# Kernel optimization log

Measured on AMD Instinct MI355X. Metric: run time of the kernel, lower is better.

The kernel has to match this reference:

```python
import jax, jax.numpy as jnp
import numpy as np

B, T, F, U, M, OUT = 2048, 16, 512, 512, 8, 3
DELTA_T = 0.04
EPS = 1e-07


def setup_inputs() -> dict:
    key = jax.random.key(0)
    ks = jax.random.split(key, 6)
    s_in = 1.0 / np.sqrt(F + U)
    s_u = 1.0 / np.sqrt(U)
    return {
        "x": jax.random.normal(ks[0], (B, T, F), dtype=jnp.float32),
        "W_r": jax.random.normal(ks[1], (F + U, U * M), dtype=jnp.float32) * s_in,
        "b_r": jnp.zeros((U * M,), dtype=jnp.float32),
        "W_q": jax.random.normal(ks[2], (F + U, U), dtype=jnp.float32) * s_in,
        "b_q": jnp.zeros((U,), dtype=jnp.float32),
        "W_s": jax.random.normal(ks[3], (F + U, U * M), dtype=jnp.float32) * s_in,
        "b_s": jnp.zeros((U * M,), dtype=jnp.float32),
        "W_o": jax.random.normal(ks[4], (U, OUT), dtype=jnp.float32) * s_u,
        "b_o": jnp.zeros((OUT,), dtype=jnp.float32),
    }


def _ln_tau_table():
    # tau_i = 10^(i/2)  =>  ln tau_i = i * 0.5 * ln(10)
    return (jnp.arange(M, dtype=jnp.float32) * (0.5 * np.log(10.0)))


def reference(x, W_r, b_r, W_q, b_q, W_s, b_s, W_o, b_o):
    ln_tau = _ln_tau_table()                       # (M,)
    decay = jnp.exp(-DELTA_T / (jnp.exp(ln_tau) + EPS))  # (M,)

    def step(h_hat, x_t):
        # h_hat: (B, U, M), x_t: (B, F)
        h = h_hat.sum(axis=2)                       # (B, U)
        fi = jnp.concatenate([x_t, h], axis=1)      # (B, F+U)
        ln_r = (fi @ W_r + b_r).reshape(-1, U, M)
        r = jax.nn.softmax(-jnp.square(ln_r - ln_tau), axis=2)
        ctx = jnp.sum(r * h_hat, axis=2)            # (B, U)
        q = jnp.tanh(jnp.concatenate([x_t, ctx], axis=1) @ W_q + b_q)[:, :, None]
        ln_s = (fi @ W_s + b_s).reshape(-1, U, M)
        s = jax.nn.softmax(-jnp.square(ln_s - ln_tau), axis=2)
        h_hat_next = ((1.0 - s) * h_hat + s * q) * decay
        hidden = h_hat_next.sum(axis=2)             # (B, U)
        return h_hat_next, hidden

    h0 = jnp.zeros((x.shape[0], U, M), dtype=x.dtype)
    xs = jnp.swapaxes(x, 0, 1)                      # (T, B, F)
    _, hs = jax.lax.scan(step, h0, xs)              # hs: (T, B, U)
    hs = jnp.swapaxes(hs, 0, 1)                     # (B, T, U)
    out = hs @ W_o + b_o                            # (B, T, OUT)
    return out
```

## Files before the change

### kernel.cpp

```cpp
#include <hip/hip_runtime.h>
#include <math.h>

#define B_ 2048
#define T_ 16
#define F_ 512
#define U_ 512
#define M_ 8

typedef _Float16 half8 __attribute__((ext_vector_type(8)));
typedef float f32x4 __attribute__((ext_vector_type(4)));

__device__ __forceinline__ void load_lds16(const _Float16* gsrc, _Float16* lds) {
    __builtin_amdgcn_global_load_lds(
        (const __attribute__((address_space(1))) void*)gsrc,
        (__attribute__((address_space(3))) void*)lds, 16, 0, 0);
}

#define BAR() __builtin_amdgcn_s_barrier()
#define LGKM0() asm volatile("s_waitcnt lgkmcnt(0)" ::: "memory")
#define VMW(n) asm volatile("s_waitcnt vmcnt(" #n ")" ::: "memory")
#define MFMA16(a, b, c) __builtin_amdgcn_mfma_f32_16x16x32_f16(a, b, c, 0, 0, 0)

struct Decay8 { float d[8]; };

__global__ __launch_bounds__(256) void cast_x_kernel(const float* __restrict__ in,
                                                     _Float16* __restrict__ out) {
    long i = (long)blockIdx.x * 256 + threadIdx.x;
    const f32x4* p = (const f32x4*)in;
    f32x4 a = p[i * 2], b = p[i * 2 + 1];
    half8 v;
    v[0] = (_Float16)a[0]; v[1] = (_Float16)a[1]; v[2] = (_Float16)a[2]; v[3] = (_Float16)a[3];
    v[4] = (_Float16)b[0]; v[5] = (_Float16)b[1]; v[6] = (_Float16)b[2]; v[7] = (_Float16)b[3];
    ((half8*)out)[i] = v;
}

__global__ __launch_bounds__(256) void transpose_cast_kernel(const float* __restrict__ W,
                                                             _Float16* __restrict__ Wt,
                                                             int K, int N) {
    __shared__ float tile[32][33];
    int n0 = blockIdx.x * 32, k0 = blockIdx.y * 32;
    int tx = threadIdx.x, ty = threadIdx.y;
    #pragma unroll
    for (int i = 0; i < 32; i += 8)
        tile[ty + i][tx] = W[(long)(k0 + ty + i) * N + n0 + tx];
    __syncthreads();
    #pragma unroll
    for (int i = 0; i < 32; i += 8)
        Wt[(long)(n0 + ty + i) * K + k0 + tx] = (_Float16)tile[tx][ty + i];
}

__global__ __launch_bounds__(256) void transpose_cast_perm_kernel(const float* __restrict__ W,
                                                                  _Float16* __restrict__ Wt,
                                                                  int rowbase) {
    const int K = 1024, N = 4096;
    __shared__ float tile[32][33];
    int n0 = blockIdx.x * 32, k0 = blockIdx.y * 32;
    int tx = threadIdx.x, ty = threadIdx.y;
    #pragma unroll
    for (int i = 0; i < 32; i += 8)
        tile[ty + i][tx] = W[(long)(k0 + ty + i) * N + n0 + tx];
    __syncthreads();
    #pragma unroll
    for (int i = 0; i < 32; i += 8) {
        int nl = n0 + ty + i;
        int u = nl >> 3, m = nl & 7;
        int nn = ((u >> 4) << 7) + (m << 4) + (u & 15);
        Wt[(long)(rowbase + nn) * K + k0 + tx] = (_Float16)tile[tx][ty + i];
    }
}

__global__ __launch_bounds__(512, 2) void gemm1_fused_kernel(
    const _Float16* __restrict__ A0, long lda0,
    const _Float16* __restrict__ A1, long lda1,
    const _Float16* __restrict__ Wt,
    const float* __restrict__ b_r, const float* __restrict__ b_s,
    const _Float16* __restrict__ h_hat,
    _Float16* __restrict__ ctx,
    _Float16* __restrict__ s_buf) {
    constexpr int NT = 16;
    const float LT = 1.1512925464970228f;
    __shared__ __align__(16) _Float16 As[2][256 * 64];
    __shared__ __align__(16) _Float16 Bs[2][256 * 64];
    const int tid = threadIdx.x;
    const int lane = tid & 63;
    const int wave = tid >> 6;
    const int wm = wave >> 1, wn = wave & 1;
    const int l15 = lane & 15, lhi = lane >> 4, swz = lane & 7;
    const int g0 = (lhi ^ swz) * 8;
    const int g1 = ((lhi + 4) ^ swz) * 8;
    const int srow = tid >> 3;
    const int sg = (tid & 7) ^ (srow & 7);
    const int ldsdst = wave * 64 * 8;
    const long m0 = (long)blockIdx.y * 256;
    const long n0 = (long)blockIdx.x * 256;

#define STAGE_A(kt_, buf_, r_) do {                                             \
        int kt__ = (kt_);                                                       \
        const _Float16* s_; long lda_; int kofs_;                               \
        if (kt__ < 8) { s_ = A0; lda_ = lda0; kofs_ = kt__ * 64; }              \
        else          { s_ = A1; lda_ = lda1; kofs_ = kt__ * 64 - 512; }        \
        load_lds16(s_ + (m0 + (r_) * 64 + srow) * lda_ + kofs_ + sg * 8,        \
                   &As[buf_][(r_) * 4096 + ldsdst]);                            \
    } while (0)
#define STAGE_B(kt_, buf_, r_)                                                  \
        load_lds16(Wt + (n0 + (r_) * 64 + srow) * 1024 + (kt_) * 64 + sg * 8,   \
                   &Bs[buf_][(r_) * 4096 + ldsdst])

    f32x4 acc[4][8] = {};

    #pragma unroll
    for (int r = 0; r < 4; ++r) STAGE_A(0, 0, r);
    #pragma unroll
    for (int r = 0; r < 4; ++r) STAGE_B(0, 0, r);
    #pragma unroll
    for (int r = 0; r < 4; ++r) STAGE_A(1, 1, r);
    STAGE_B(1, 1, 0); STAGE_B(1, 1, 2);
    VMW(6);
    BAR();

    #pragma unroll 1
    for (int t = 0; t < NT; ++t) {
        const int cur = t & 1, nxt = cur ^ 1;
        const _Float16* Ac = &As[cur][0];
        const _Float16* Bc = &Bs[cur][0];
        half8 af[4][2], bfa[2][2], bfb[2][2];

        #pragma unroll
        for (int i = 0; i < 4; ++i) {
            const _Float16* p = Ac + (wm * 64 + i * 16 + l15) * 64;
            af[i][0] = *(const half8*)(p + g0);
            af[i][1] = *(const half8*)(p + g1);
        }
        #pragma unroll
        for (int j = 0; j < 2; ++j) {
            const _Float16* p = Bc + (wn * 128 + j * 16 + l15) * 64;
            bfa[j][0] = *(const half8*)(p + g0);
            bfa[j][1] = *(const half8*)(p + g1);
        }
        if (t + 1 < NT) { STAGE_B(t + 1, nxt, 1); STAGE_B(t + 1, nxt, 3); }
        BAR(); LGKM0();
        __builtin_amdgcn_s_setprio(1);
        #pragma unroll
        for (int i = 0; i < 4; ++i)
            #pragma unroll
            for (int j = 0; j < 2; ++j) {
                acc[i][j] = MFMA16(af[i][0], bfa[j][0], acc[i][j]);
                acc[i][j] = MFMA16(af[i][1], bfa[j][1], acc[i][j]);
            }
        __builtin_amdgcn_s_setprio(0);
        BAR();

        #pragma unroll
        for (int j = 0; j < 2; ++j) {
            const _Float16* p = Bc + (wn * 128 + (2 + j) * 16 + l15) * 64;
            bfb[j][0] = *(const half8*)(p + g0);
            bfb[j][1] = *(const half8*)(p + g1);
        }
        if (t + 2 < NT) { STAGE_A(t + 2, cur, 0); STAGE_A(t + 2, cur, 1); }
        BAR(); LGKM0();
        __builtin_amdgcn_s_setprio(1);
        #pragma unroll
        for (int i = 0; i < 4; ++i)
            #pragma unroll
            for (int j = 0; j < 2; ++j) {
                acc[i][2 + j] = MFMA16(af[i][0], bfb[j][0], acc[i][2 + j]);
                acc[i][2 + j] = MFMA16(af[i][1], bfb[j][1], acc[i][2 + j]);
            }
        __builtin_amdgcn_s_setprio(0);
        BAR();

        #pragma unroll
        for (int j = 0; j < 2; ++j) {
            const _Float16* p = Bc + (wn * 128 + (4 + j) * 16 + l15) * 64;
            bfa[j][0] = *(const half8*)(p + g0);
            bfa[j][1] = *(const half8*)(p + g1);
        }
        if (t + 2 < NT) { STAGE_A(t + 2, cur, 2); STAGE_A(t + 2, cur, 3); }
        BAR(); LGKM0();
        __builtin_amdgcn_s_setprio(1);
        #pragma unroll
        for (int i = 0; i < 4; ++i)
            #pragma unroll
            for (int j = 0; j < 2; ++j) {
                acc[i][4 + j] = MFMA16(af[i][0], bfa[j][0], acc[i][4 + j]);
                acc[i][4 + j] = MFMA16(af[i][1], bfa[j][1], acc[i][4 + j]);
            }
        __builtin_amdgcn_s_setprio(0);
        BAR();

        #pragma unroll
        for (int j = 0; j < 2; ++j) {
            const _Float16* p = Bc + (wn * 128 + (6 + j) * 16 + l15) * 64;
            bfb[j][0] = *(const half8*)(p + g0);
            bfb[j][1] = *(const half8*)(p + g1);
        }
        if (t + 2 < NT) { STAGE_B(t + 2, cur, 0); STAGE_B(t + 2, cur, 2); }
        LGKM0();
        __builtin_amdgcn_s_setprio(1);
        #pragma unroll
        for (int i = 0; i < 4; ++i)
            #pragma unroll
            for (int j = 0; j < 2; ++j) {
                acc[i][6 + j] = MFMA16(af[i][0], bfb[j][0], acc[i][6 + j]);
                acc[i][6 + j] = MFMA16(af[i][1], bfb[j][1], acc[i][6 + j]);
            }
        __builtin_amdgcn_s_setprio(0);
        if (t + 2 < NT)      { VMW(6); }
        else if (t + 1 < NT) { VMW(0); }
        BAR();
    }

    const int r4 = lhi * 4;
    const int panel = (int)(n0 >> 7) + wn;
    const bool is_r = panel < 32;
    const int u = (is_r ? panel : panel - 32) * 16 + l15;
    const float* bias = is_r ? b_r : b_s;
    f32x4 bl0 = *(const f32x4*)(bias + u * 8);
    f32x4 bl1 = *(const f32x4*)(bias + u * 8 + 4);

    #pragma unroll
    for (int i = 0; i < 4; ++i) {
        #pragma unroll
        for (int r = 0; r < 4; ++r) {
            long m = m0 + wm * 64 + i * 16 + r4 + r;
            float z[8]; float zmax = -1e30f;
            #pragma unroll
            for (int j = 0; j < 8; ++j) {
                float v = acc[i][j][r] + (j < 4 ? bl0[j] : bl1[j - 4]);
                float d = v - (float)j * LT;
                z[j] = -d * d;
                zmax = fmaxf(zmax, z[j]);
            }
            float e[8]; float se = 0.f;
            #pragma unroll
            for (int j = 0; j < 8; ++j) { e[j] = __expf(z[j] - zmax); se += e[j]; }
            float inv = 1.f / se;
            if (is_r) {
                half8 hh = *(const half8*)(h_hat + m * 4096 + u * 8);
                float c = 0.f;
                #pragma unroll
                for (int j = 0; j < 8; ++j) c += e[j] * (float)hh[j];
                ctx[m * 512 + u] = (_Float16)(c * inv);
            } else {
                half8 sv;
                #pragma unroll
                for (int j = 0; j < 8; ++j) sv[j] = (_Float16)(e[j] * inv);
                *(half8*)(s_buf + m * 4096 + u * 8) = sv;
            }
        }
    }
#undef STAGE_A
#undef STAGE_B
}

__global__ __launch_bounds__(256) void gemm2_fused_kernel(
    const _Float16* __restrict__ A0, long lda0,
    const _Float16* __restrict__ A1, long lda1,
    const _Float16* __restrict__ Wt,
    const float* __restrict__ bias,
    const _Float16* __restrict__ s_buf,
    _Float16* __restrict__ h_hat,
    _Float16* __restrict__ hs_t,
    Decay8 dec) {
    constexpr int BM = 64, BN = 64, FM = 2, FN = 2;
    __shared__ __align__(16) _Float16 As[BM * 64];
    __shared__ __align__(16) _Float16 Bs[BN * 64];
    const int tid = threadIdx.x;
    const int lane = tid & 63;
    const int wave = tid >> 6;
    const int wm = wave >> 1, wn = wave & 1;
    const long m0 = (long)blockIdx.y * BM;
    const long n0 = (long)blockIdx.x * BN;

    f32x4 acc[FM][FN] = {};

    for (int kt = 0; kt < 16; ++kt) {
        const _Float16* Asrc; long lda; int kofs;
        if (kt < 8) { Asrc = A0; lda = lda0; kofs = kt * 64; }
        else        { Asrc = A1; lda = lda1; kofs = kt * 64 - 512; }
        #pragma unroll
        for (int c = 0; c < 2; ++c) {
            int idx = c * 256 + tid;
            int row = idx >> 3, g = idx & 7;
            int gsrc = g ^ (row & 7);
            load_lds16(Asrc + (m0 + row) * lda + kofs + gsrc * 8,
                       As + (c * 256 + (wave << 6)) * 8);
        }
        #pragma unroll
        for (int c = 0; c < 2; ++c) {
            int idx = c * 256 + tid;
            int row = idx >> 3, g = idx & 7;
            int gsrc = g ^ (row & 7);
            load_lds16(Wt + (n0 + row) * 1024 + kt * 64 + gsrc * 8,
                       Bs + (c * 256 + (wave << 6)) * 8);
        }
        __syncthreads();
        #pragma unroll
        for (int ks = 0; ks < 2; ++ks) {
            half8 af[FM], bf[FN];
            #pragma unroll
            for (int i = 0; i < FM; ++i) {
                int row = wm * 32 + i * 16 + (lane & 15);
                int g = ks * 4 + (lane >> 4);
                int gs = g ^ (row & 7);
                af[i] = *(const half8*)(As + row * 64 + gs * 8);
            }
            #pragma unroll
            for (int j = 0; j < FN; ++j) {
                int row = wn * 32 + j * 16 + (lane & 15);
                int g = ks * 4 + (lane >> 4);
                int gs = g ^ (row & 7);
                bf[j] = *(const half8*)(Bs + row * 64 + gs * 8);
            }
            #pragma unroll
            for (int i = 0; i < FM; ++i)
                #pragma unroll
                for (int j = 0; j < FN; ++j)
                    acc[i][j] = MFMA16(af[i], bf[j], acc[i][j]);
        }
        __syncthreads();
    }

    const int r4 = (lane >> 4) * 4;
    const int c16 = lane & 15;
    #pragma unroll
    for (int i = 0; i < FM; ++i) {
        #pragma unroll
        for (int j = 0; j < FN; ++j) {
            #pragma unroll
            for (int r = 0; r < 4; ++r) {
                long b = m0 + wm * 32 + i * 16 + r4 + r;
                long u = n0 + wn * 32 + j * 16 + c16;
                float q = tanhf(acc[i][j][r] + bias[u]);
                half8 s8 = *(const half8*)(s_buf + b * 4096 + u * 8);
                half8 h8 = *(const half8*)(h_hat + b * 4096 + u * 8);
                half8 hn;
                float hval = 0.f;
                #pragma unroll
                for (int m = 0; m < 8; ++m) {
                    float sm = (float)s8[m];
                    float x = ((1.f - sm) * (float)h8[m] + sm * q) * dec.d[m];
                    hn[m] = (_Float16)x;
                    hval += x;
                }
                *(half8*)(h_hat + b * 4096 + u * 8) = hn;
                hs_t[b * 512 + u] = (_Float16)hval;
            }
        }
    }
}

__global__ __launch_bounds__(64) void out_proj_kernel(const _Float16* __restrict__ hs,
                                                      const float* __restrict__ W_o,
                                                      const float* __restrict__ b_o,
                                                      float* __restrict__ out) {
    const int bt = blockIdx.x;
    const int t = bt >> 11, b = bt & 2047;
    const int lane = threadIdx.x;
    half8 v = *(const half8*)(hs + ((long)t * 2048 + b) * 512 + lane * 8);
    float p0 = 0.f, p1 = 0.f, p2 = 0.f;
    #pragma unroll
    for (int m = 0; m < 8; ++m) {
        float hv = (float)v[m];
        int u = lane * 8 + m;
        p0 += hv * W_o[u * 3 + 0];
        p1 += hv * W_o[u * 3 + 1];
        p2 += hv * W_o[u * 3 + 2];
    }
    #pragma unroll
    for (int s = 32; s > 0; s >>= 1) {
        p0 += __shfl_down(p0, s);
        p1 += __shfl_down(p1, s);
        p2 += __shfl_down(p2, s);
    }
    if (lane == 0) {
        long o = ((long)b * T_ + t) * 3;
        out[o + 0] = p0 + b_o[0];
        out[o + 1] = p1 + b_o[1];
        out[o + 2] = p2 + b_o[2];
    }
}

extern "C" void kernel_launch(void* const* d_in, const int* in_sizes, int n_in,
                              void* d_out, int out_size, void* d_ws, size_t ws_size,
                              hipStream_t stream) {
    const float* x   = (const float*)d_in[0];
    const float* W_r = (const float*)d_in[1];
    const float* b_r = (const float*)d_in[2];
    const float* W_q = (const float*)d_in[3];
    const float* b_q = (const float*)d_in[4];
    const float* W_s = (const float*)d_in[5];
    const float* b_s = (const float*)d_in[6];
    const float* W_o = (const float*)d_in[7];
    const float* b_o = (const float*)d_in[8];
    float* out = (float*)d_out;

    char* ws = (char*)d_ws;
    size_t off = 0;
    _Float16* x_h   = (_Float16*)(ws + off); off += (size_t)B_ * T_ * F_ * 2;
    _Float16* Wrs_t = (_Float16*)(ws + off); off += (size_t)8192 * 1024 * 2;
    _Float16* Wq_t  = (_Float16*)(ws + off); off += (size_t)512 * 1024 * 2;
    _Float16* s_buf = (_Float16*)(ws + off); off += (size_t)B_ * 4096 * 2;
    _Float16* h_hat = (_Float16*)(ws + off); off += (size_t)B_ * 4096 * 2;
    _Float16* ctx_h = (_Float16*)(ws + off); off += (size_t)B_ * U_ * 2;
    _Float16* hs    = (_Float16*)(ws + off); off += (size_t)T_ * B_ * U_ * 2;
    _Float16* zbuf  = (_Float16*)(ws + off); off += (size_t)B_ * U_ * 2;
    if (ws_size < off) return;

    hipMemsetAsync(h_hat, 0, (size_t)B_ * 4096 * 2, stream);
    hipMemsetAsync(zbuf, 0, (size_t)B_ * U_ * 2, stream);

    cast_x_kernel<<<dim3((B_ * T_ * F_) / (256 * 8)), 256, 0, stream>>>(x, x_h);
    transpose_cast_perm_kernel<<<dim3(4096 / 32, 1024 / 32), dim3(32, 8), 0, stream>>>(W_r, Wrs_t, 0);
    transpose_cast_perm_kernel<<<dim3(4096 / 32, 1024 / 32), dim3(32, 8), 0, stream>>>(W_s, Wrs_t, 4096);
    transpose_cast_kernel<<<dim3(512 / 32, 1024 / 32), dim3(32, 8), 0, stream>>>(W_q, Wq_t, 1024, 512);

    Decay8 dec;
    for (int m = 0; m < 8; ++m) {
        float lt = (float)m * 1.1512925464970228f;
        dec.d[m] = expf(-0.04f / (expf(lt) + 1e-7f));
    }

    for (int t = 0; t < T_; ++t) {
        const _Float16* hprev = (t == 0) ? zbuf : hs + (size_t)(t - 1) * B_ * U_;
        gemm1_fused_kernel<<<dim3(8192 / 256, B_ / 256), 512, 0, stream>>>(
            x_h + (long)t * F_, (long)T_ * F_, hprev, U_, Wrs_t,
            b_r, b_s, h_hat, ctx_h, s_buf);
        gemm2_fused_kernel<<<dim3(512 / 64, B_ / 64), 256, 0, stream>>>(
            x_h + (long)t * F_, (long)T_ * F_, ctx_h, U_, Wq_t,
            b_q, s_buf, h_hat, hs + (size_t)t * B_ * U_, dec);
    }
    out_proj_kernel<<<dim3(B_ * T_), 64, 0, stream>>>(hs, W_o, b_o, out);
    (void)in_sizes; (void)n_in; (void)out_size;
}
```

Before: 1.029 ms.

## Double-buffer gemm2 LDS tiles and use 8 waves per block

Restructures the q-projection GEMM kernel so global-to-LDS loads for the next K tile are issued before computing the current one, using two LDS buffers and a vmcnt wait instead of full syncs around each load. The block grows from 256 to 512 threads, so each wave owns a 16x32 sub-tile instead of 32x32, which lowers per-wave register use and raises the wave count. The aim is to hide global load latency in this small K-looped GEMM. The trade-off is more LDS per block and less MFMA work per wave relative to its LDS reads.

```diff
diff --git a/kernel.cpp b/kernel.cpp
--- a/kernel.cpp
+++ b/kernel.cpp
@@ -253,7 +253,7 @@
 #undef STAGE_B
 }
 
-__global__ __launch_bounds__(256) void gemm2_fused_kernel(
+__global__ __launch_bounds__(512) void gemm2_fused_kernel(
     const _Float16* __restrict__ A0, long lda0,
     const _Float16* __restrict__ A1, long lda1,
     const _Float16* __restrict__ Wt,
@@ -262,90 +262,86 @@
     _Float16* __restrict__ h_hat,
     _Float16* __restrict__ hs_t,
     Decay8 dec) {
-    constexpr int BM = 64, BN = 64, FM = 2, FN = 2;
-    __shared__ __align__(16) _Float16 As[BM * 64];
-    __shared__ __align__(16) _Float16 Bs[BN * 64];
+    constexpr int NT = 16;
+    __shared__ __align__(16) _Float16 As[2][64 * 64];
+    __shared__ __align__(16) _Float16 Bs[2][64 * 64];
     const int tid = threadIdx.x;
     const int lane = tid & 63;
     const int wave = tid >> 6;
     const int wm = wave >> 1, wn = wave & 1;
-    const long m0 = (long)blockIdx.y * BM;
-    const long n0 = (long)blockIdx.x * BN;
-
-    f32x4 acc[FM][FN] = {};
-
-    for (int kt = 0; kt < 16; ++kt) {
-        const _Float16* Asrc; long lda; int kofs;
-        if (kt < 8) { Asrc = A0; lda = lda0; kofs = kt * 64; }
-        else        { Asrc = A1; lda = lda1; kofs = kt * 64 - 512; }
-        #pragma unroll
-        for (int c = 0; c < 2; ++c) {
-            int idx = c * 256 + tid;
-            int row = idx >> 3, g = idx & 7;
-            int gsrc = g ^ (row & 7);
-            load_lds16(Asrc + (m0 + row) * lda + kofs + gsrc * 8,
-                       As + (c * 256 + (wave << 6)) * 8);
-        }
-        #pragma unroll
-        for (int c = 0; c < 2; ++c) {
-            int idx = c * 256 + tid;
-            int row = idx >> 3, g = idx & 7;
-            int gsrc = g ^ (row & 7);
-            load_lds16(Wt + (n0 + row) * 1024 + kt * 64 + gsrc * 8,
-                       Bs + (c * 256 + (wave << 6)) * 8);
-        }
-        __syncthreads();
-        #pragma unroll
-        for (int ks = 0; ks < 2; ++ks) {
-            half8 af[FM], bf[FN];
-            #pragma unroll
-            for (int i = 0; i < FM; ++i) {
-                int row = wm * 32 + i * 16 + (lane & 15);
-                int g = ks * 4 + (lane >> 4);
-                int gs = g ^ (row & 7);
-                af[i] = *(const half8*)(As + row * 64 + gs * 8);
-            }
-            #pragma unroll
-            for (int j = 0; j < FN; ++j) {
-                int row = wn * 32 + j * 16 + (lane & 15);
-                int g = ks * 4 + (lane >> 4);
-                int gs = g ^ (row & 7);
-                bf[j] = *(const half8*)(Bs + row * 64 + gs * 8);
-            }
-            #pragma unroll
-            for (int i = 0; i < FM; ++i)
-                #pragma unroll
-                for (int j = 0; j < FN; ++j)
-                    acc[i][j] = MFMA16(af[i], bf[j], acc[i][j]);
-        }
-        __syncthreads();
-    }
-
-    const int r4 = (lane >> 4) * 4;
-    const int c16 = lane & 15;
-    #pragma unroll
-    for (int i = 0; i < FM; ++i) {
-        #pragma unroll
-        for (int j = 0; j < FN; ++j) {
-            #pragma unroll
-            for (int r = 0; r < 4; ++r) {
-                long b = m0 + wm * 32 + i * 16 + r4 + r;
-                long u = n0 + wn * 32 + j * 16 + c16;
-                float q = tanhf(acc[i][j][r] + bias[u]);
-                half8 s8 = *(const half8*)(s_buf + b * 4096 + u * 8);
-                half8 h8 = *(const half8*)(h_hat + b * 4096 + u * 8);
-                half8 hn;
-                float hval = 0.f;
-                #pragma unroll
-                for (int m = 0; m < 8; ++m) {
-                    float sm = (float)s8[m];
-                    float x = ((1.f - sm) * (float)h8[m] + sm * q) * dec.d[m];
-                    hn[m] = (_Float16)x;
-                    hval += x;
-                }
-                *(half8*)(h_hat + b * 4096 + u * 8) = hn;
-                hs_t[b * 512 + u] = (_Float16)hval;
-            }
+    const int l15 = lane & 15, lhi = lane >> 4, swz = lane & 7;
+    const int g0 = (lhi ^ swz) * 8;
+    const int g1 = ((lhi + 4) ^ swz) * 8;
+    const int srow = tid >> 3;
+    const int sg = (tid & 7) ^ (srow & 7);
+    const long m0 = (long)blockIdx.y * 64;
+    const long n0 = (long)blockIdx.x * 64;
+
+#define STAGE2(kt_, buf_) do {                                                  \
+        int kt__ = (kt_);                                                       \
+        const _Float16* s_; long lda_; int kofs_;                               \
+        if (kt__ < 8) { s_ = A0; lda_ = lda0; kofs_ = kt__ * 64; }              \
+        else          { s_ = A1; lda_ = lda1; kofs_ = kt__ * 64 - 512; }        \
+        load_lds16(s_ + (m0 + srow) * lda_ + kofs_ + sg * 8,                    \
+                   &As[buf_][wave * 512]);                                      \
+        load_lds16(Wt + (n0 + srow) * 1024 + kt__ * 64 + sg * 8,                \
+                   &Bs[buf_][wave * 512]);                                      \
+    } while (0)
+
+    f32x4 acc[2] = {};
+
+    STAGE2(0, 0);
+    #pragma unroll 1
+    for (int kt = 0; kt < NT; ++kt) {
+        const int cur = kt & 1;
+        if (kt + 1 < NT) { STAGE2(kt + 1, cur ^ 1); VMW(2); }
+        else             { VMW(0); }
+        BAR();
+        const _Float16* Ac = &As[cur][0];
+        const _Float16* Bc = &Bs[cur][0];
+        half8 af[2], bf[2][2];
+        {
+            const _Float16* p = Ac + (wm * 16 + l15) * 64;
+            af[0] = *(const half8*)(p + g0);
+            af[1] = *(const half8*)(p + g1);
+        }
+        #pragma unroll
+        for (int j = 0; j < 2; ++j) {
+            const _Float16* p = Bc + (wn * 32 + j * 16 + l15) * 64;
+            bf[j][0] = *(const half8*)(p + g0);
+            bf[j][1] = *(const half8*)(p + g1);
+        }
+        LGKM0();
+        #pragma unroll
+        for (int j = 0; j < 2; ++j) {
+            acc[j] = MFMA16(af[0], bf[j][0], acc[j]);
+            acc[j] = MFMA16(af[1], bf[j][1], acc[j]);
+        }
+        BAR();
+    }
+#undef STAGE2
+
+    const int r4 = lhi * 4;
+    #pragma unroll
+    for (int j = 0; j < 2; ++j) {
+        #pragma unroll
+        for (int r = 0; r < 4; ++r) {
+            long b = m0 + wm * 16 + r4 + r;
+            long u = n0 + wn * 32 + j * 16 + l15;
+            float q = tanhf(acc[j][r] + bias[u]);
+            half8 s8 = *(const half8*)(s_buf + b * 4096 + u * 8);
+            half8 h8 = *(const half8*)(h_hat + b * 4096 + u * 8);
+            half8 hn;
+            float hval = 0.f;
+            #pragma unroll
+            for (int m = 0; m < 8; ++m) {
+                float sm = (float)s8[m];
+                float x = ((1.f - sm) * (float)h8[m] + sm * q) * dec.d[m];
+                hn[m] = (_Float16)x;
+                hval += x;
+            }
+            *(half8*)(h_hat + b * 4096 + u * 8) = hn;
+            hs_t[b * 512 + u] = (_Float16)hval;
         }
     }
 }
@@ -426,7 +422,7 @@
         gemm1_fused_kernel<<<dim3(8192 / 256, B_ / 256), 512, 0, stream>>>(
             x_h + (long)t * F_, (long)T_ * F_, hprev, U_, Wrs_t,
             b_r, b_s, h_hat, ctx_h, s_buf);
-        gemm2_fused_kernel<<<dim3(512 / 64, B_ / 64), 256, 0, stream>>>(
+        gemm2_fused_kernel<<<dim3(512 / 64, B_ / 64), 512, 0, stream>>>(
             x_h + (long)t * F_, (long)T_ * F_, ctx_h, U_, Wq_t,
             b_q, s_buf, h_hat, hs + (size_t)t * B_ * U_, dec);
     }
```

After: 1.006 ms. 2.3% less time.
